# Optimization experiments

Measured on AMD Instinct MI355X. Metric: run time of the kernel, lower is better.

Reference implementation:

```python
import jax, jax.numpy as jnp
import numpy as np

B, T, C = 2, 2048, 1024
H, KH, HD = 16, 4, 64
E, TOPK, I = 8, 2, 1024
GATE = 32
EPS = 1.1920929e-07  # torch F.rms_norm default eps = fp32 machine eps


def rmsnorm(v):
    return v * jax.lax.rsqrt(jnp.mean(v * v, axis=-1, keepdims=True) + EPS)


def rope(v, cos, sin):
    d = v.shape[-1] // 2
    a, b = v[..., :d], v[..., d:]
    return jnp.concatenate([a * cos + b * sin, -a * sin + b * cos], axis=-1)


def setup_inputs() -> dict:
    key = jax.random.key(0)
    ks = jax.random.split(key, 14)
    rn = lambda i, shape, s=1.0: jax.random.normal(ks[i], shape, jnp.float32) * s
    inv_freq = 1.0 / (10000.0 ** (np.arange(HD // 2, dtype=np.float64) / (HD // 2)))
    ang = np.outer(np.arange(T), inv_freq)
    cos = jnp.asarray(np.cos(ang), jnp.float32)[None, :, None, :]
    sin = jnp.asarray(np.sin(ang), jnp.float32)[None, :, None, :]
    w = 0.02
    return {
        'x': rn(0, (B, T, C)),
        've': rn(1, (B, T, KH * HD)),
        'cos': cos,
        'sin': sin,
        'Wq': rn(2, (C, H * HD), w),
        'Wk': rn(3, (KH * HD, C), w),
        'Wv': rn(4, (KH * HD, C), w),
        'Wo': rn(5, (C, C), w),
        've_gate_W': rn(6, (KH, GATE), w),
        'router_W': rn(7, (E, C), w),
        'balance_bias': jnp.zeros((E,), jnp.float32),
        'shared_fc_W': rn(8, (I, C), w),
        'shared_proj_W': rn(9, (C, I), w),
        'exp_fc_W': rn(10, (E, I, C), w),
        'exp_proj_W': rn(11, (E, C, I), w),
        'window_size': T,
    }


def reference(x, ve, cos, sin, Wq, Wk, Wv, Wo, ve_gate_W, router_W, balance_bias,
              shared_fc_W, shared_proj_W, exp_fc_W, exp_proj_W, window_size):
    # ---- attention branch: x = x + attn(norm(x)) ----
    h = rmsnorm(x)
    q = (h @ Wq.T).reshape(B, T, H, HD)
    k = (h @ Wk.T).reshape(B, T, KH, HD)
    v = (h @ Wv.T).reshape(B, T, KH, HD)
    # value-embedding gate (has_ve true for this layer)
    gate = 2.0 * jax.nn.sigmoid(h[..., :GATE] @ ve_gate_W.T)  # [B,T,KH]
    v = v + gate[..., None] * ve.reshape(B, T, KH, HD)
    q, k = rope(q, cos, sin), rope(k, cos, sin)
    q, k = rmsnorm(q), rmsnorm(k)
    g = H // KH
    kr = jnp.repeat(k, g, axis=2)  # GQA expansion [B,T,H,HD]
    vr = jnp.repeat(v, g, axis=2)
    scores = jnp.einsum('bthd,bshd->bhts', q, kr) / jnp.sqrt(jnp.float32(HD))
    ti = jnp.arange(T)[:, None]
    si = jnp.arange(T)[None, :]
    mask = (si <= ti) & (si > ti - window_size)  # causal + sliding window
    scores = jnp.where(mask, scores, -jnp.inf)
    p = jax.nn.softmax(scores, axis=-1)
    y = jnp.einsum('bhts,bshd->bthd', p, vr).reshape(B, T, C)
    x = x + y @ Wo.T

    # ---- MoE branch: x = x + shared(norm(x)) + routed(norm(x)) ----
    h2 = rmsnorm(x)
    shared = jnp.square(jax.nn.relu(h2 @ shared_fc_W.T)) @ shared_proj_W.T
    flat = h2.reshape(-1, C)  # [N,C]
    logits = flat @ router_W.T  # [N,E]
    sc = jax.nn.sigmoid(logits)
    _, topi = jax.lax.top_k(sc + balance_bias, TOPK)  # select on biased scores
    topw = jnp.take_along_axis(sc, topi, axis=1)      # weights from raw scores
    topw = topw / (jnp.sum(topw, axis=-1, keepdims=True) + 1e-20)
    N = flat.shape[0]
    combine = jnp.zeros((N, E), flat.dtype).at[jnp.arange(N)[:, None], topi].add(topw)
    # dense grouped compute, mathematically equal to gather/scatter dispatch
    he = jnp.square(jax.nn.relu(jnp.einsum('nc,eic->eni', flat, exp_fc_W)))
    oe = jnp.einsum('eni,eci->enc', he, exp_proj_W)
    routed = jnp.einsum('enc,ne->nc', oe, combine).reshape(B, T, C)
    return x + shared + routed
```

## Files before the change

### kernel.cpp

```cpp
#include <hip/hip_runtime.h>

#define TT 2048
#define CC 1024
#define NTOK 4096
#define EPSF 1.1920929e-07f

typedef unsigned short u16;
typedef short bf16x8 __attribute__((ext_vector_type(8)));
typedef u16 u16x4 __attribute__((ext_vector_type(4)));
typedef float f32x4 __attribute__((ext_vector_type(4)));

__device__ __forceinline__ u16 f2b(float f) {
  union { float f; unsigned u; } v; v.f = f;
  unsigned r = v.u + 0x7FFFu + ((v.u >> 16) & 1u);
  return (u16)(r >> 16);
}
__device__ __forceinline__ float b2f(u16 u) {
  union { unsigned u; float f; } v; v.u = ((unsigned)u) << 16;
  return v.f;
}
__device__ __forceinline__ void gload16(const u16* g, u16* l) {
  __builtin_amdgcn_global_load_lds(
      (const __attribute__((address_space(1))) void*)g,
      (__attribute__((address_space(3))) void*)l, 16, 0, 0);
}
__device__ __forceinline__ bf16x8 ldsf(const u16* s, int row, int kseg) {
  return *(const bf16x8*)(s + (row << 6) + ((kseg ^ (row & 7)) << 3));
}

__global__ __launch_bounds__(256) void cvt_split4_k(const float* __restrict__ p0,
                                                    const float* __restrict__ p1,
                                                    const float* __restrict__ p2,
                                                    const float* __restrict__ p3,
                                                    u16* __restrict__ h0, u16* __restrict__ l0,
                                                    u16* __restrict__ h1, u16* __restrict__ l1,
                                                    u16* __restrict__ h2, u16* __restrict__ l2,
                                                    u16* __restrict__ h3, u16* __restrict__ l3) {
  const int sizes[4] = {131072, 32768, 32768, 131072};
  int seg = blockIdx.y;
  int i = blockIdx.x * 256 + threadIdx.x;
  if (i >= sizes[seg]) return;
  const float* in = seg == 0 ? p0 : seg == 1 ? p1 : seg == 2 ? p2 : p3;
  u16* ho = seg == 0 ? h0 : seg == 1 ? h1 : seg == 2 ? h2 : h3;
  u16* lo = seg == 0 ? l0 : seg == 1 ? l1 : seg == 2 ? l2 : l3;
  i *= 8;
  float v[8];
  *(float4*)v = *(const float4*)(in + i);
  *(float4*)(v + 4) = *(const float4*)(in + i + 4);
  u16 h[8], l[8];
#pragma unroll
  for (int j = 0; j < 8; ++j) {
    h[j] = f2b(v[j]);
    l[j] = f2b(v[j] - b2f(h[j]));
  }
  *(bf16x8*)(ho + i) = *(bf16x8*)h;
  *(bf16x8*)(lo + i) = *(bf16x8*)l;
}

__global__ __launch_bounds__(256) void rmsnorm_split_k(const float* __restrict__ in,
                                                       u16* __restrict__ hio,
                                                       u16* __restrict__ loo,
                                                       const float* __restrict__ gW,
                                                       float* __restrict__ gates) {
  const int rowi = blockIdx.x;
  const int t = threadIdx.x;
  float4 v = ((const float4*)(in + (size_t)rowi * CC))[t];
  float ss = v.x * v.x + v.y * v.y + v.z * v.z + v.w * v.w;
#pragma unroll
  for (int off = 32; off; off >>= 1) ss += __shfl_down(ss, off, 64);
  __shared__ float red[4];
  __shared__ float hshare[32];
  if ((t & 63) == 0) red[t >> 6] = ss;
  __syncthreads();
  float tot = red[0] + red[1] + red[2] + red[3];
  float sc = rsqrtf(tot * (1.0f / CC) + EPSF);
  float o[4] = {v.x * sc, v.y * sc, v.z * sc, v.w * sc};
  u16 h[4], l[4];
#pragma unroll
  for (int j = 0; j < 4; ++j) {
    h[j] = f2b(o[j]);
    l[j] = f2b(o[j] - b2f(h[j]));
  }
  *(u16x4*)(hio + (size_t)rowi * CC + t * 4) = *(u16x4*)h;
  *(u16x4*)(loo + (size_t)rowi * CC + t * 4) = *(u16x4*)l;
  if (t < 8) *(float4*)&hshare[t << 2] = *(float4*)o;
  __syncthreads();
  if (t < 4) {
    const float* gw = gW + (t << 5);
    float dot = 0.f;
#pragma unroll
    for (int j = 0; j < 32; ++j) dot += hshare[j] * gw[j];
    gates[(rowi << 2) + t] = 2.f / (1.f + __expf(-dot));
  }
}

__global__ __launch_bounds__(256) void rmsnorm_logits_k(const float* __restrict__ in,
                                                        u16* __restrict__ b16o,
                                                        const float* __restrict__ rW,
                                                        float* __restrict__ logits) {
  const int rowi = blockIdx.x;
  const int t = threadIdx.x;
  float4 v = ((const float4*)(in + (size_t)rowi * CC))[t];
  float ss = v.x * v.x + v.y * v.y + v.z * v.z + v.w * v.w;
#pragma unroll
  for (int off = 32; off; off >>= 1) ss += __shfl_down(ss, off, 64);
  __shared__ float red[4];
  __shared__ float red2[8][4];
  if ((t & 63) == 0) red[t >> 6] = ss;
  __syncthreads();
  float tot = red[0] + red[1] + red[2] + red[3];
  float sc = rsqrtf(tot * (1.0f / CC) + EPSF);
  float o[4] = {v.x * sc, v.y * sc, v.z * sc, v.w * sc};
  u16 h[4] = {f2b(o[0]), f2b(o[1]), f2b(o[2]), f2b(o[3])};
  *(u16x4*)(b16o + (size_t)rowi * CC + t * 4) = *(u16x4*)h;
  const float* rwp = rW + (t << 2);
  float part[8];
#pragma unroll
  for (int e = 0; e < 8; ++e) {
    const float* w = rwp + (e << 10);
    part[e] = o[0] * w[0] + o[1] * w[1] + o[2] * w[2] + o[3] * w[3];
  }
  const int wid = t >> 6;
#pragma unroll
  for (int e = 0; e < 8; ++e) {
    float p = part[e];
#pragma unroll
    for (int off = 32; off; off >>= 1) p += __shfl_down(p, off, 64);
    if ((t & 63) == 0) red2[e][wid] = p;
  }
  __syncthreads();
  if (t < 8) logits[rowi * 8 + t] = red2[t][0] + red2[t][1] + red2[t][2] + red2[t][3];
}

template <int MODE>
__global__ __launch_bounds__(256) void gemm_bf_k(
    const u16* __restrict__ A, const u16* __restrict__ A2,
    const u16* __restrict__ Wt, const u16* __restrict__ W2,
    const u16* __restrict__ Wk1, const u16* __restrict__ Wk2,
    const u16* __restrict__ Wv1, const u16* __restrict__ Wv2,
    float* __restrict__ Cf, u16* __restrict__ Cb,
    u16* __restrict__ Ck, u16* __restrict__ Cv,
    const float* __restrict__ addv, int N, int K,
    const int* __restrict__ offsets, const int* __restrict__ counts,
    const int* __restrict__ tok_idx, const float* __restrict__ tok_w,
    const float* __restrict__ cosb, const float* __restrict__ sinb,
    const float* __restrict__ gates, const float* __restrict__ vein) {
  constexpr bool SPLIT = (MODE == 6 || MODE == 11);
  __shared__ __align__(16) u16 Asw[SPLIT ? 16384 : 8192];
  __shared__ __align__(16) u16 Bsw[SPLIT ? 8192 : 4096];
  const int t = threadIdx.x;
  const int lane = t & 63;
  const int l15 = lane & 15, hi = lane >> 4;
  const int wave = t >> 6;
  const int e = blockIdx.z;
  const int mt = blockIdx.y << 7;
  const int bn = blockIdx.x << 6;
  int base = 0, cnt = 0;
  if (MODE == 4 || MODE == 5) {
    cnt = (e == 8) ? NTOK : counts[e];
    if (mt >= cnt) return;
    base = (e == 8) ? 8192 : offsets[e];
  }
  const int r8 = t >> 3;
  const int ksg = (t & 7) ^ (r8 & 7);
  const u16* asrc[4];
  const u16* bsrc[2];
  const u16* asrc2[4];
  const u16* bsrc2[2];
  const u16* W1p = Wt;
  if (MODE == 4 || MODE == 5) W1p = (e == 8) ? Wk1 : Wt + ((size_t)e << 20);
  const u16* W2p = W2;
  int wrow = bn;
  if (MODE == 11) {
    if (bn >= 1280)      { W1p = Wv1; W2p = Wv2; wrow = bn - 1280; }
    else if (bn >= 1024) { W1p = Wk1; W2p = Wk2; wrow = bn - 1024; }
  }
#pragma unroll
  for (int g = 0; g < 4; ++g) {
    int rl = (g << 5) + r8;
    int arow;
    if (MODE == 4) {
      int rr = mt + rl; if (rr > cnt - 1) rr = cnt - 1;
      arow = (e == 8) ? rr : tok_idx[base + rr];
    } else if (MODE == 5) {
      int rr = mt + rl; if (rr > cnt - 1) rr = cnt - 1;
      arow = base + rr;
    } else {
      arow = mt + rl;
    }
    size_t ao = (size_t)arow * K + (ksg << 3);
    asrc[g] = A + ao;
    if (SPLIT) asrc2[g] = A2 + ao;
  }
#pragma unroll
  for (int g = 0; g < 2; ++g) {
    size_t bo = (size_t)(wrow + (g << 5) + r8) * K + (ksg << 3);
    bsrc[g] = W1p + bo;
    if (SPLIT) bsrc2[g] = W2p + bo;
  }
  f32x4 acc[2][4] = {};
  const int nkt = K >> 6;
  for (int kt = 0; kt < nkt; ++kt) {
    __syncthreads();
    const int ko = kt << 6;
#pragma unroll
    for (int g = 0; g < 4; ++g) {
      int co = ((g << 8) + t) << 3;
      gload16(asrc[g] + ko, &Asw[co]);
      if (SPLIT) gload16(asrc2[g] + ko, &Asw[8192 + co]);
    }
#pragma unroll
    for (int g = 0; g < 2; ++g) {
      int co = ((g << 8) + t) << 3;
      gload16(bsrc[g] + ko, &Bsw[co]);
      if (SPLIT) gload16(bsrc2[g] + ko, &Bsw[4096 + co]);
    }
    __syncthreads();
#pragma unroll
    for (int kk = 0; kk < 2; ++kk) {
      bf16x8 ah[2], bh[4];
#pragma unroll
      for (int mi = 0; mi < 2; ++mi)
        ah[mi] = ldsf(Asw, (wave << 5) + (mi << 4) + l15, (kk << 2) + hi);
#pragma unroll
      for (int nj = 0; nj < 4; ++nj)
        bh[nj] = ldsf(Bsw, (nj << 4) + l15, (kk << 2) + hi);
#pragma unroll
      for (int mi = 0; mi < 2; ++mi)
#pragma unroll
        for (int nj = 0; nj < 4; ++nj)
          acc[mi][nj] = __builtin_amdgcn_mfma_f32_16x16x32_bf16(ah[mi], bh[nj], acc[mi][nj], 0, 0, 0);
      if (SPLIT) {
        bf16x8 al[2], bl[4];
#pragma unroll
        for (int mi = 0; mi < 2; ++mi)
          al[mi] = ldsf(Asw + 8192, (wave << 5) + (mi << 4) + l15, (kk << 2) + hi);
#pragma unroll
        for (int nj = 0; nj < 4; ++nj)
          bl[nj] = ldsf(Bsw + 4096, (nj << 4) + l15, (kk << 2) + hi);
#pragma unroll
        for (int mi = 0; mi < 2; ++mi)
#pragma unroll
          for (int nj = 0; nj < 4; ++nj) {
            acc[mi][nj] = __builtin_amdgcn_mfma_f32_16x16x32_bf16(ah[mi], bl[nj], acc[mi][nj], 0, 0, 0);
            acc[mi][nj] = __builtin_amdgcn_mfma_f32_16x16x32_bf16(al[mi], bh[nj], acc[mi][nj], 0, 0, 0);
          }
      }
    }
  }
  if (MODE == 11) {
    if (bn < 1280) {
      u16* outp = (bn < 1024) ? Cb : Ck;
      const int stride = (bn < 1024) ? 1024 : 256;
      const int cbase = (bn < 1024) ? bn : (bn - 1024);
#pragma unroll
      for (int mi = 0; mi < 2; ++mi) {
#pragma unroll
        for (int r = 0; r < 4; ++r) {
          int row = mt + (wave << 5) + (mi << 4) + (hi << 2) + r;
          int tpos = row & (TT - 1);
          const float* cp = cosb + (tpos << 5);
          const float* sp = sinb + (tpos << 5);
          float c0 = cp[l15], s0 = sp[l15];
          float c1 = cp[16 + l15], s1 = sp[16 + l15];
          float a0 = acc[mi][0][r], a1 = acc[mi][1][r];
          float b0 = acc[mi][2][r], b1 = acc[mi][3][r];
          float r00 = a0 * c0 + b0 * s0;
          float r01 = a1 * c1 + b1 * s1;
          float r10 = b0 * c0 - a0 * s0;
          float r11 = b1 * c1 - a1 * s1;
          float ss = r00 * r00 + r01 * r01 + r10 * r10 + r11 * r11;
          ss += __shfl_xor(ss, 1, 64); ss += __shfl_xor(ss, 2, 64);
          ss += __shfl_xor(ss, 4, 64); ss += __shfl_xor(ss, 8, 64);
          float scn = rsqrtf(ss * (1.f / 64.f) + EPSF);
          u16* qp = outp + (size_t)row * stride + cbase;
          qp[l15]      = f2b(r00 * scn);
          qp[16 + l15] = f2b(r01 * scn);
          qp[32 + l15] = f2b(r10 * scn);
          qp[48 + l15] = f2b(r11 * scn);
        }
      }
    } else {
      const int cbase = bn - 1280;
      const int kvh = cbase >> 6;
#pragma unroll
      for (int mi = 0; mi < 2; ++mi) {
#pragma unroll
        for (int r = 0; r < 4; ++r) {
          int row = mt + (wave << 5) + (mi << 4) + (hi << 2) + r;
          float g = gates[(row << 2) + kvh];
          const float* vep = vein + ((size_t)row << 8) + cbase;
          size_t vb_base = ((size_t)(((row >> 11) << 2) + kvh) << 17) + (row & (TT - 1));
#pragma unroll
          for (int nj = 0; nj < 4; ++nj) {
            int d = (nj << 4) + l15;
            Cv[vb_base + ((size_t)d << 11)] = f2b(acc[mi][nj][r] + g * vep[d]);
          }
        }
      }
    }
    return;
  }
#pragma unroll
  for (int mi = 0; mi < 2; ++mi) {
#pragma unroll
    for (int r = 0; r < 4; ++r) {
      int rl = (wave << 5) + (mi << 4) + (hi << 2) + r;
      if (MODE == 4 || MODE == 5) {
        int rr = mt + rl;
        if (rr >= cnt) continue;
        if (MODE == 4) {
          size_t ro = (size_t)(base + rr) * N;
#pragma unroll
          for (int nj = 0; nj < 4; ++nj) {
            float v = acc[mi][nj][r];
            v = v > 0.f ? v * v : 0.f;
            Cb[ro + bn + (nj << 4) + l15] = f2b(v);
          }
        } else {
          int tok = (e == 8) ? rr : tok_idx[base + rr];
          float w = (e == 8) ? 1.0f : tok_w[base + rr];
          size_t ro = (size_t)tok * N;
#pragma unroll
          for (int nj = 0; nj < 4; ++nj)
            atomicAdd(&Cf[ro + bn + (nj << 4) + l15], acc[mi][nj][r] * w);
        }
      } else {
        size_t ro = (size_t)(mt + rl) * N;
        float* outp = (float*)Cb;
#pragma unroll
        for (int nj = 0; nj < 4; ++nj) {
          int col = bn + (nj << 4) + l15;
          float v = acc[mi][nj][r] + addv[ro + col];
          Cf[ro + col] = v;
          outp[ro + col] = v;
        }
      }
    }
  }
}

__global__ __launch_bounds__(256) void attn_mfma_k(const u16* __restrict__ qb,
                                                   const u16* __restrict__ kb,
                                                   const u16* __restrict__ vbT,
                                                   u16* __restrict__ yh,
                                                   u16* __restrict__ yl,
                                                   const int* __restrict__ wszp,
                                                   float* __restrict__ po,
                                                   float* __restrict__ pml,
                                                   const float* __restrict__ cSfc,
                                                   const float* __restrict__ cSproj,
                                                   const float* __restrict__ cEfc,
                                                   const float* __restrict__ cEproj,
                                                   u16* __restrict__ oSfc,
                                                   u16* __restrict__ oSproj,
                                                   u16* __restrict__ oEfc,
                                                   u16* __restrict__ oEproj) {
  const int z = blockIdx.z;
  const int b = z >> 1, seg = z & 1;
  const int kvh = blockIdx.y;
  const int qf = 127 - (int)blockIdx.x;
  const int t = threadIdx.x;
  if (qf < 64 && seg) {
    const int cid = (((b << 2) + kvh) << 6) + ((int)blockIdx.x - 64);
    int chunk = cid * 4608 + t;
#pragma unroll
    for (int it = 0; it < 18; ++it, chunk += 256) {
      const float* in;
      u16* ou;
      int loc;
      if (chunk < 131072)       { in = cSfc;   ou = oSfc;   loc = chunk; }
      else if (chunk < 262144)  { in = cSproj; ou = oSproj; loc = chunk - 131072; }
      else if (chunk < 1310720) { in = cEfc;   ou = oEfc;   loc = chunk - 262144; }
      else                      { in = cEproj; ou = oEproj; loc = chunk - 1310720; }
      size_t i = (size_t)loc * 8;
      float4 a = *(const float4*)(in + i);
      float4 bb = *(const float4*)(in + i + 4);
      u16 r[8] = {f2b(a.x), f2b(a.y), f2b(a.z), f2b(a.w),
                  f2b(bb.x), f2b(bb.y), f2b(bb.z), f2b(bb.w)};
      *(bf16x8*)(ou + i) = *(bf16x8*)r;
    }
    return;
  }
  const int Wn = *wszp;
  const int lane = t & 63, wave = t >> 6;
  const int h = (kvh << 2) + wave;
  const int l15 = lane & 15, hi = lane >> 4;

  __shared__ __align__(16) u16 Klds[2 * 4096];
  __shared__ __align__(16) u16 Vt[2 * 4096];
  __shared__ __align__(16) u16 Plds[4][16 * 64];

  const int qrow0 = qf << 4;
  const int diag = qrow0 >> 6;
  int lo = qrow0 - Wn + 1;
  const int kt0f = lo > 0 ? (lo >> 6) : 0;
  int kt0 = kt0f, ktend = diag;
  if (qf >= 64) {
    int nt = diag - kt0f + 1;
    int mid = kt0f + (nt >> 1);
    if (seg == 0) ktend = mid - 1; else kt0 = mid;
  }

  bf16x8 aQ0, aQ1;
  {
    const u16* qp = qb + ((size_t)((b << 11) + qrow0 + l15) << 10) + (h << 6) + (hi << 3);
    aQ0 = *(const bf16x8*)qp;
    aQ1 = *(const bf16x8*)(qp + 32);
  }
  f32x4 o[4] = {};
  float mrow[4] = {-INFINITY, -INFINITY, -INFINITY, -INFINITY};
  float lrow[4] = {0.f, 0.f, 0.f, 0.f};

  const int kr0 = t >> 3, kc = t & 7;
  const u16* vbase = vbT + ((size_t)((b << 2) + kvh) << 17);

#pragma unroll
  for (int i = 0; i < 2; ++i) {
    int row = kr0 + (i << 5);
    int scol = (kc ^ (row & 7)) << 3;
    gload16(kb + ((size_t)((b << 11) + (kt0 << 6) + row) << 8) + (kvh << 6) + scol,
            &Klds[(t << 3) + (i << 11)]);
    gload16(vbase + ((size_t)row << 11) + (kt0 << 6) + scol,
            &Vt[(t << 3) + (i << 11)]);
  }
  int cur = 0;

  for (int kt = kt0; kt <= ktend; ++kt) {
    __syncthreads();
    if (kt + 1 <= ktend) {
      const int nb = (cur ^ 1) << 12;
#pragma unroll
      for (int i = 0; i < 2; ++i) {
        int row = kr0 + (i << 5);
        int scol = (kc ^ (row & 7)) << 3;
        gload16(kb + ((size_t)((b << 11) + ((kt + 1) << 6) + row) << 8) + (kvh << 6) + scol,
                &Klds[nb + (t << 3) + (i << 11)]);
        gload16(vbase + ((size_t)row << 11) + ((kt + 1) << 6) + scol,
                &Vt[nb + (t << 3) + (i << 11)]);
      }
    }
    const u16* Kb = Klds + (cur << 12);
    const u16* Vb = Vt + (cur << 12);

    float sv[4][4];
    __builtin_amdgcn_s_setprio(1);
#pragma unroll
    for (int kb4 = 0; kb4 < 4; ++kb4) {
      f32x4 S = {0.f, 0.f, 0.f, 0.f};
      bf16x8 B0 = ldsf(Kb, (kb4 << 4) + l15, hi);
      bf16x8 B1 = ldsf(Kb, (kb4 << 4) + l15, 4 + hi);
      S = __builtin_amdgcn_mfma_f32_16x16x32_bf16(aQ0, B0, S, 0, 0, 0);
      S = __builtin_amdgcn_mfma_f32_16x16x32_bf16(aQ1, B1, S, 0, 0, 0);
#pragma unroll
      for (int r = 0; r < 4; ++r) sv[kb4][r] = S[r] * 0.125f;
    }
    __builtin_amdgcn_s_setprio(0);
    if (kt == diag || kt == kt0f) {
#pragma unroll
      for (int kb4 = 0; kb4 < 4; ++kb4) {
        int key = (kt << 6) + (kb4 << 4) + l15;
#pragma unroll
        for (int r = 0; r < 4; ++r) {
          int qg = qrow0 + (hi << 2) + r;
          if (!(key <= qg && key > qg - Wn)) sv[kb4][r] = -INFINITY;
        }
      }
    }

    float scl[4], pv[4][4];
#pragma unroll
    for (int r = 0; r < 4; ++r) {
      float mt2 = fmaxf(fmaxf(sv[0][r], sv[1][r]), fmaxf(sv[2][r], sv[3][r]));
      mt2 = fmaxf(mt2, __shfl_xor(mt2, 1, 64));
      mt2 = fmaxf(mt2, __shfl_xor(mt2, 2, 64));
      mt2 = fmaxf(mt2, __shfl_xor(mt2, 4, 64));
      mt2 = fmaxf(mt2, __shfl_xor(mt2, 8, 64));
      float mn = fmaxf(fmaxf(mrow[r], mt2), -1e30f);
      float sc = __expf(mrow[r] - mn);
      float rs = 0.f;
#pragma unroll
      for (int kb4 = 0; kb4 < 4; ++kb4) {
        float p = __expf(sv[kb4][r] - mn);
        pv[kb4][r] = p;
        rs += p;
      }
      rs += __shfl_xor(rs, 1, 64);
      rs += __shfl_xor(rs, 2, 64);
      rs += __shfl_xor(rs, 4, 64);
      rs += __shfl_xor(rs, 8, 64);
      mrow[r] = mn;
      lrow[r] = lrow[r] * sc + rs;
      scl[r] = sc;
    }

#pragma unroll
    for (int kb4 = 0; kb4 < 4; ++kb4)
#pragma unroll
      for (int r = 0; r < 4; ++r) {
        int row16 = (hi << 2) + r;
        int seg2 = (kb4 << 1) + (l15 >> 3);
        Plds[wave][(row16 << 6) + ((seg2 ^ (row16 & 7)) << 3) + (l15 & 7)] = f2b(pv[kb4][r]);
      }
#pragma unroll
    for (int df = 0; df < 4; ++df) {
      f32x4 t4 = o[df];
      t4[0] *= scl[0]; t4[1] *= scl[1]; t4[2] *= scl[2]; t4[3] *= scl[3];
      o[df] = t4;
    }
    __builtin_amdgcn_s_setprio(1);
#pragma unroll
    for (int ks = 0; ks < 2; ++ks) {
      bf16x8 Ap = ldsf(Plds[wave], l15, (ks << 2) + hi);
#pragma unroll
      for (int df = 0; df < 4; ++df) {
        bf16x8 Bv = ldsf(Vb, (df << 4) + l15, (ks << 2) + hi);
        o[df] = __builtin_amdgcn_mfma_f32_16x16x32_bf16(Ap, Bv, o[df], 0, 0, 0);
      }
    }
    __builtin_amdgcn_s_setprio(0);
    cur ^= 1;
  }

  if (qf < 64) {
    float inv[4];
#pragma unroll
    for (int r = 0; r < 4; ++r) inv[r] = lrow[r] > 0.f ? 1.f / lrow[r] : 0.f;
#pragma unroll
    for (int r = 0; r < 4; ++r) {
      size_t rbase = ((size_t)((b << 11) + qrow0 + (hi << 2) + r) << 10) + (h << 6) + l15;
#pragma unroll
      for (int df = 0; df < 4; ++df) {
        float fo = o[df][r] * inv[r];
        u16 hv = f2b(fo);
        yh[rbase + (df << 4)] = hv;
        yl[rbase + (df << 4)] = f2b(fo - b2f(hv));
      }
    }
  } else {
    const int sidx = (b << 1) + seg;
    const int prow0 = qrow0 - 1024;
#pragma unroll
    for (int r = 0; r < 4; ++r) {
      size_t pbase = ((size_t)(sidx * 1024 + prow0 + (hi << 2) + r) << 10) + (h << 6) + l15;
#pragma unroll
      for (int df = 0; df < 4; ++df) po[pbase + (df << 4)] = o[df][r];
    }
    if (l15 == 0) {
#pragma unroll
      for (int r = 0; r < 4; ++r) {
        size_t mb = ((size_t)(sidx * 1024 + prow0 + (hi << 2) + r) << 5) + (h << 1);
        pml[mb] = mrow[r];
        pml[mb + 1] = lrow[r];
      }
    }
  }
}

__global__ __launch_bounds__(256) void combine_k(const float* __restrict__ po,
                                                 const float* __restrict__ pml,
                                                 u16* __restrict__ yh,
                                                 u16* __restrict__ yl) {
  const int prow = blockIdx.x, b = blockIdx.y;
  const int t = threadIdx.x;
  const int h = t >> 4, d0 = (t & 15) << 2;
  const int s0 = b << 1, s1 = s0 + 1;
  size_t i0 = ((size_t)(s0 * 1024 + prow) << 5) + (h << 1);
  size_t i1 = ((size_t)(s1 * 1024 + prow) << 5) + (h << 1);
  float m0 = pml[i0], l0 = pml[i0 + 1];
  float m1 = pml[i1], l1 = pml[i1 + 1];
  float m = fmaxf(m0, m1);
  float sc0 = __expf(m0 - m), sc1 = __expf(m1 - m);
  float l = l0 * sc0 + l1 * sc1;
  float inv = l > 0.f ? 1.f / l : 0.f;
  size_t o0 = ((size_t)(s0 * 1024 + prow) << 10) + (h << 6) + d0;
  size_t o1 = ((size_t)(s1 * 1024 + prow) << 10) + (h << 6) + d0;
  float4 a = *(const float4*)&po[o0];
  float4 c = *(const float4*)&po[o1];
  float y0 = (a.x * sc0 + c.x * sc1) * inv;
  float y1 = (a.y * sc0 + c.y * sc1) * inv;
  float y2 = (a.z * sc0 + c.z * sc1) * inv;
  float y3 = (a.w * sc0 + c.w * sc1) * inv;
  u16 hv[4] = {f2b(y0), f2b(y1), f2b(y2), f2b(y3)};
  u16 lv[4] = {f2b(y0 - b2f(hv[0])), f2b(y1 - b2f(hv[1])),
               f2b(y2 - b2f(hv[2])), f2b(y3 - b2f(hv[3]))};
  size_t rbase = ((size_t)((b << 11) + 1024 + prow) << 10) + (h << 6) + d0;
  *(u16x4*)(yh + rbase) = *(u16x4*)hv;
  *(u16x4*)(yl + rbase) = *(u16x4*)lv;
}

__global__ __launch_bounds__(256) void topk_k(const float* __restrict__ logits,
                                              const float* __restrict__ bias,
                                              int* __restrict__ topi,
                                              float* __restrict__ topw,
                                              int* __restrict__ counts) {
  int n = blockIdx.x * 256 + threadIdx.x;
  if (n >= NTOK) return;
  float sc[8], sel[8];
#pragma unroll
  for (int e2 = 0; e2 < 8; ++e2) {
    float sg = 1.f / (1.f + __expf(-logits[n * 8 + e2]));
    sc[e2] = sg;
    sel[e2] = sg + bias[e2];
  }
  int i1 = 0; float b1 = sel[0];
#pragma unroll
  for (int j = 1; j < 8; ++j) if (sel[j] > b1) { b1 = sel[j]; i1 = j; }
  int i2 = -1; float b2 = -INFINITY;
#pragma unroll
  for (int j = 0; j < 8; ++j) if (j != i1 && sel[j] > b2) { b2 = sel[j]; i2 = j; }
  float w1 = sc[i1], w2 = sc[i2];
  float invs = 1.f / (w1 + w2 + 1e-20f);
  topi[n * 2] = i1; topi[n * 2 + 1] = i2;
  topw[n * 2] = w1 * invs; topw[n * 2 + 1] = w2 * invs;
  atomicAdd(&counts[i1], 1);
  atomicAdd(&counts[i2], 1);
}

__global__ void scan_k(const int* __restrict__ counts, int* __restrict__ offsets) {
  if (threadIdx.x == 0 && blockIdx.x == 0) {
    int s = 0;
    for (int e2 = 0; e2 < 8; ++e2) { offsets[e2] = s; s += counts[e2]; }
    offsets[8] = s;
  }
}

__global__ __launch_bounds__(256) void scatter_k(const int* __restrict__ topi,
                                                 const float* __restrict__ topw,
                                                 const int* __restrict__ offsets,
                                                 int* __restrict__ counts2,
                                                 int* __restrict__ tok_idx,
                                                 float* __restrict__ tok_w) {
  int n = blockIdx.x * 256 + threadIdx.x;
  if (n >= NTOK) return;
  for (int kk = 0; kk < 2; ++kk) {
    int e2 = topi[n * 2 + kk];
    int slot = atomicAdd(&counts2[e2], 1);
    int p = offsets[e2] + slot;
    tok_idx[p] = n;
    tok_w[p] = topw[n * 2 + kk];
  }
}

extern "C" void kernel_launch(void* const* d_in, const int* in_sizes, int n_in,
                              void* d_out, int out_size, void* d_ws, size_t ws_size,
                              hipStream_t stream) {
  const float* x = (const float*)d_in[0];
  const float* ve = (const float*)d_in[1];
  const float* cosb = (const float*)d_in[2];
  const float* sinb = (const float*)d_in[3];
  const float* Wq = (const float*)d_in[4];
  const float* Wk = (const float*)d_in[5];
  const float* Wv = (const float*)d_in[6];
  const float* Wo = (const float*)d_in[7];
  const float* gW = (const float*)d_in[8];
  const float* routerW = (const float*)d_in[9];
  const float* bias = (const float*)d_in[10];
  const float* Wsfc = (const float*)d_in[11];
  const float* Wsproj = (const float*)d_in[12];
  const float* Wefc = (const float*)d_in[13];
  const float* Weproj = (const float*)d_in[14];
  const int* wsz = (const int*)d_in[15];
  float* out = (float*)d_out;
  char* WS = (char*)d_ws;

  u16* Wefc_b   = (u16*)(WS + 0);
  u16* Weproj_b = (u16*)(WS + 16777216);
  u16* Wsfc_b   = (u16*)(WS + 33554432);
  u16* Wsproj_b = (u16*)(WS + 35651584);
  u16* Wq_hi    = (u16*)(WS + 37748736);
  u16* Wq_lo    = (u16*)(WS + 39845888);
  u16* Wk_hi    = (u16*)(WS + 41943040);
  u16* Wk_lo    = (u16*)(WS + 42467328);
  u16* Wv_hi    = (u16*)(WS + 42991616);
  u16* Wv_lo    = (u16*)(WS + 43515904);
  u16* Wo_hi    = (u16*)(WS + 44040192);
  u16* Wo_lo    = (u16*)(WS + 46137344);
  u16* h_hi     = (u16*)(WS + 48234496);
  u16* h_lo     = (u16*)(WS + 56623104);
  u16* qb       = (u16*)(WS + 65011712);
  u16* kb       = (u16*)(WS + 73400320);
  u16* vb       = (u16*)(WS + 75497472);
  u16* y_hi     = (u16*)(WS + 77594624);
  u16* y_lo     = (u16*)(WS + 85983232);
  float* po     = (float*)(WS + 48234496);
  float* x2     = (float*)(WS + 48234496);
  u16* h2_b     = (u16*)(WS + 85983232);
  u16* he_b     = (u16*)(WS + 48234496);
  float* gates  = (float*)(WS + 94371840);
  float* logits = (float*)(WS + 94437376);
  int* meta     = (int*)(WS + 94568448);
  int* counts   = meta;
  int* counts2  = meta + 8;
  int* offsets  = meta + 16;
  int* topi     = meta + 32;
  float* topw   = (float*)(meta + 8224);
  int* tok_idx  = meta + 16416;
  float* tok_w  = (float*)(meta + 24608);
  float* pml    = (float*)(WS + 94703616);

  hipMemsetAsync(counts, 0, 16 * sizeof(int), stream);

  cvt_split4_k<<<dim3(512, 4), 256, 0, stream>>>(Wq, Wk, Wv, Wo,
      Wq_hi, Wq_lo, Wk_hi, Wk_lo, Wv_hi, Wv_lo, Wo_hi, Wo_lo);

  rmsnorm_split_k<<<NTOK, 256, 0, stream>>>(x, h_hi, h_lo, gW, gates);
  gemm_bf_k<11><<<dim3(24, 32), 256, 0, stream>>>(
      h_hi, h_lo, Wq_hi, Wq_lo, Wk_hi, Wk_lo, Wv_hi, Wv_lo,
      nullptr, qb, kb, vb, nullptr, 1536, 1024,
      nullptr, nullptr, nullptr, nullptr, cosb, sinb, gates, ve);
  attn_mfma_k<<<dim3(128, 4, 4), 256, 0, stream>>>(qb, kb, vb, y_hi, y_lo, wsz, po, pml,
      Wsfc, Wsproj, Wefc, Weproj, Wsfc_b, Wsproj_b, Wefc_b, Weproj_b);
  combine_k<<<dim3(1024, 2), 256, 0, stream>>>(po, pml, y_hi, y_lo);
  gemm_bf_k<6><<<dim3(16, 32), 256, 0, stream>>>(
      y_hi, y_lo, Wo_hi, Wo_lo, nullptr, nullptr, nullptr, nullptr,
      x2, (u16*)out, nullptr, nullptr, x, 1024, 1024,
      nullptr, nullptr, nullptr, nullptr, nullptr, nullptr, nullptr, nullptr);
  rmsnorm_logits_k<<<NTOK, 256, 0, stream>>>(x2, h2_b, routerW, logits);
  topk_k<<<16, 256, 0, stream>>>(logits, bias, topi, topw, counts);
  scan_k<<<1, 64, 0, stream>>>(counts, offsets);
  scatter_k<<<16, 256, 0, stream>>>(topi, topw, offsets, counts2, tok_idx, tok_w);
  gemm_bf_k<4><<<dim3(16, 32, 9), 256, 0, stream>>>(
      h2_b, nullptr, Wefc_b, nullptr, Wsfc_b, nullptr, nullptr, nullptr,
      nullptr, he_b, nullptr, nullptr, nullptr, 1024, 1024,
      offsets, counts, tok_idx, nullptr, nullptr, nullptr, nullptr, nullptr);
  gemm_bf_k<5><<<dim3(16, 32, 9), 256, 0, stream>>>(
      he_b, nullptr, Weproj_b, nullptr, Wsproj_b, nullptr, nullptr, nullptr,
      out, nullptr, nullptr, nullptr, nullptr, 1024, 1024,
      offsets, counts, tok_idx, tok_w, nullptr, nullptr, nullptr, nullptr);
}
```

Baseline: 390.4 us.

## Fuse weight split-conversion into rmsnorm launch and halve M-tile for split GEMMs

The separate fp32-to-bf16 hi/lo weight conversion kernel is merged into the rmsnorm kernel as extra blocks, removing one launch and letting the two independent jobs run concurrently. For the split-precision GEMMs (QKV with RoPE and the Wo projection), the M tile shrinks from 128 to 64 rows, so each wave computes one 16-row MFMA slice and the grid doubles. This is meant to raise occupancy and CU coverage for these small GEMMs (768 and 512 blocks before), at the cost of less reuse of the B tile per block.

```diff
diff --git a/kernel.cpp b/kernel.cpp
--- a/kernel.cpp
+++ b/kernel.cpp
@@ -28,42 +28,43 @@
   return *(const bf16x8*)(s + (row << 6) + ((kseg ^ (row & 7)) << 3));
 }
 
-__global__ __launch_bounds__(256) void cvt_split4_k(const float* __restrict__ p0,
-                                                    const float* __restrict__ p1,
-                                                    const float* __restrict__ p2,
-                                                    const float* __restrict__ p3,
-                                                    u16* __restrict__ h0, u16* __restrict__ l0,
-                                                    u16* __restrict__ h1, u16* __restrict__ l1,
-                                                    u16* __restrict__ h2, u16* __restrict__ l2,
-                                                    u16* __restrict__ h3, u16* __restrict__ l3) {
-  const int sizes[4] = {131072, 32768, 32768, 131072};
-  int seg = blockIdx.y;
-  int i = blockIdx.x * 256 + threadIdx.x;
-  if (i >= sizes[seg]) return;
-  const float* in = seg == 0 ? p0 : seg == 1 ? p1 : seg == 2 ? p2 : p3;
-  u16* ho = seg == 0 ? h0 : seg == 1 ? h1 : seg == 2 ? h2 : h3;
-  u16* lo = seg == 0 ? l0 : seg == 1 ? l1 : seg == 2 ? l2 : l3;
-  i *= 8;
-  float v[8];
-  *(float4*)v = *(const float4*)(in + i);
-  *(float4*)(v + 4) = *(const float4*)(in + i + 4);
-  u16 h[8], l[8];
-#pragma unroll
-  for (int j = 0; j < 8; ++j) {
-    h[j] = f2b(v[j]);
-    l[j] = f2b(v[j] - b2f(h[j]));
-  }
-  *(bf16x8*)(ho + i) = *(bf16x8*)h;
-  *(bf16x8*)(lo + i) = *(bf16x8*)l;
-}
-
 __global__ __launch_bounds__(256) void rmsnorm_split_k(const float* __restrict__ in,
                                                        u16* __restrict__ hio,
                                                        u16* __restrict__ loo,
                                                        const float* __restrict__ gW,
-                                                       float* __restrict__ gates) {
-  const int rowi = blockIdx.x;
+                                                       float* __restrict__ gates,
+                                                       const float* __restrict__ p0,
+                                                       const float* __restrict__ p1,
+                                                       const float* __restrict__ p2,
+                                                       const float* __restrict__ p3,
+                                                       u16* __restrict__ h0, u16* __restrict__ l0,
+                                                       u16* __restrict__ h1, u16* __restrict__ l1,
+                                                       u16* __restrict__ h2, u16* __restrict__ l2,
+                                                       u16* __restrict__ h3, u16* __restrict__ l3) {
+  const int bid = blockIdx.x;
   const int t = threadIdx.x;
+  if (bid >= NTOK) {
+    int chunk = (bid - NTOK) * 256 + t;
+    const float* inw; u16* ho; u16* lo2; int loc;
+    if (chunk < 131072)      { inw = p0; ho = h0; lo2 = l0; loc = chunk; }
+    else if (chunk < 163840) { inw = p1; ho = h1; lo2 = l1; loc = chunk - 131072; }
+    else if (chunk < 196608) { inw = p2; ho = h2; lo2 = l2; loc = chunk - 163840; }
+    else                     { inw = p3; ho = h3; lo2 = l3; loc = chunk - 196608; }
+    size_t i = (size_t)loc * 8;
+    float v[8];
+    *(float4*)v = *(const float4*)(inw + i);
+    *(float4*)(v + 4) = *(const float4*)(inw + i + 4);
+    u16 hh[8], ll[8];
+#pragma unroll
+    for (int j = 0; j < 8; ++j) {
+      hh[j] = f2b(v[j]);
+      ll[j] = f2b(v[j] - b2f(hh[j]));
+    }
+    *(bf16x8*)(ho + i) = *(bf16x8*)hh;
+    *(bf16x8*)(lo2 + i) = *(bf16x8*)ll;
+    return;
+  }
+  const int rowi = bid;
   float4 v = ((const float4*)(in + (size_t)rowi * CC))[t];
   float ss = v.x * v.x + v.y * v.y + v.z * v.z + v.w * v.w;
 #pragma unroll
@@ -146,14 +147,16 @@
     const float* __restrict__ cosb, const float* __restrict__ sinb,
     const float* __restrict__ gates, const float* __restrict__ vein) {
   constexpr bool SPLIT = (MODE == 6 || MODE == 11);
-  __shared__ __align__(16) u16 Asw[SPLIT ? 16384 : 8192];
+  constexpr int NAG = SPLIT ? 2 : 4;
+  constexpr int NMI = SPLIT ? 1 : 2;
+  __shared__ __align__(16) u16 Asw[8192];
   __shared__ __align__(16) u16 Bsw[SPLIT ? 8192 : 4096];
   const int t = threadIdx.x;
   const int lane = t & 63;
   const int l15 = lane & 15, hi = lane >> 4;
   const int wave = t >> 6;
   const int e = blockIdx.z;
-  const int mt = blockIdx.y << 7;
+  const int mt = blockIdx.y << (SPLIT ? 6 : 7);
   const int bn = blockIdx.x << 6;
   int base = 0, cnt = 0;
   if (MODE == 4 || MODE == 5) {
@@ -163,9 +166,9 @@
   }
   const int r8 = t >> 3;
   const int ksg = (t & 7) ^ (r8 & 7);
-  const u16* asrc[4];
+  const u16* asrc[NAG];
   const u16* bsrc[2];
-  const u16* asrc2[4];
+  const u16* asrc2[NAG];
   const u16* bsrc2[2];
   const u16* W1p = Wt;
   if (MODE == 4 || MODE == 5) W1p = (e == 8) ? Wk1 : Wt + ((size_t)e << 20);
@@ -176,7 +179,7 @@
     else if (bn >= 1024) { W1p = Wk1; W2p = Wk2; wrow = bn - 1024; }
   }
 #pragma unroll
-  for (int g = 0; g < 4; ++g) {
+  for (int g = 0; g < NAG; ++g) {
     int rl = (g << 5) + r8;
     int arow;
     if (MODE == 4) {
@@ -198,16 +201,16 @@
     bsrc[g] = W1p + bo;
     if (SPLIT) bsrc2[g] = W2p + bo;
   }
-  f32x4 acc[2][4] = {};
+  f32x4 acc[NMI][4] = {};
   const int nkt = K >> 6;
   for (int kt = 0; kt < nkt; ++kt) {
     __syncthreads();
     const int ko = kt << 6;
 #pragma unroll
-    for (int g = 0; g < 4; ++g) {
+    for (int g = 0; g < NAG; ++g) {
       int co = ((g << 8) + t) << 3;
       gload16(asrc[g] + ko, &Asw[co]);
-      if (SPLIT) gload16(asrc2[g] + ko, &Asw[8192 + co]);
+      if (SPLIT) gload16(asrc2[g] + ko, &Asw[4096 + co]);
     }
 #pragma unroll
     for (int g = 0; g < 2; ++g) {
@@ -218,28 +221,28 @@
     __syncthreads();
 #pragma unroll
     for (int kk = 0; kk < 2; ++kk) {
-      bf16x8 ah[2], bh[4];
-#pragma unroll
-      for (int mi = 0; mi < 2; ++mi)
-        ah[mi] = ldsf(Asw, (wave << 5) + (mi << 4) + l15, (kk << 2) + hi);
+      bf16x8 ah[NMI], bh[4];
+#pragma unroll
+      for (int mi = 0; mi < NMI; ++mi)
+        ah[mi] = ldsf(Asw, (SPLIT ? (wave << 4) : ((wave << 5) + (mi << 4))) + l15, (kk << 2) + hi);
 #pragma unroll
       for (int nj = 0; nj < 4; ++nj)
         bh[nj] = ldsf(Bsw, (nj << 4) + l15, (kk << 2) + hi);
 #pragma unroll
-      for (int mi = 0; mi < 2; ++mi)
+      for (int mi = 0; mi < NMI; ++mi)
 #pragma unroll
         for (int nj = 0; nj < 4; ++nj)
           acc[mi][nj] = __builtin_amdgcn_mfma_f32_16x16x32_bf16(ah[mi], bh[nj], acc[mi][nj], 0, 0, 0);
       if (SPLIT) {
-        bf16x8 al[2], bl[4];
-#pragma unroll
-        for (int mi = 0; mi < 2; ++mi)
-          al[mi] = ldsf(Asw + 8192, (wave << 5) + (mi << 4) + l15, (kk << 2) + hi);
+        bf16x8 al[NMI], bl[4];
+#pragma unroll
+        for (int mi = 0; mi < NMI; ++mi)
+          al[mi] = ldsf(Asw + 4096, (wave << 4) + l15, (kk << 2) + hi);
 #pragma unroll
         for (int nj = 0; nj < 4; ++nj)
           bl[nj] = ldsf(Bsw + 4096, (nj << 4) + l15, (kk << 2) + hi);
 #pragma unroll
-        for (int mi = 0; mi < 2; ++mi)
+        for (int mi = 0; mi < NMI; ++mi)
 #pragma unroll
           for (int nj = 0; nj < 4; ++nj) {
             acc[mi][nj] = __builtin_amdgcn_mfma_f32_16x16x32_bf16(ah[mi], bl[nj], acc[mi][nj], 0, 0, 0);
@@ -254,58 +257,52 @@
       const int stride = (bn < 1024) ? 1024 : 256;
       const int cbase = (bn < 1024) ? bn : (bn - 1024);
 #pragma unroll
-      for (int mi = 0; mi < 2; ++mi) {
-#pragma unroll
-        for (int r = 0; r < 4; ++r) {
-          int row = mt + (wave << 5) + (mi << 4) + (hi << 2) + r;
-          int tpos = row & (TT - 1);
-          const float* cp = cosb + (tpos << 5);
-          const float* sp = sinb + (tpos << 5);
-          float c0 = cp[l15], s0 = sp[l15];
-          float c1 = cp[16 + l15], s1 = sp[16 + l15];
-          float a0 = acc[mi][0][r], a1 = acc[mi][1][r];
-          float b0 = acc[mi][2][r], b1 = acc[mi][3][r];
-          float r00 = a0 * c0 + b0 * s0;
-          float r01 = a1 * c1 + b1 * s1;
-          float r10 = b0 * c0 - a0 * s0;
-          float r11 = b1 * c1 - a1 * s1;
-          float ss = r00 * r00 + r01 * r01 + r10 * r10 + r11 * r11;
-          ss += __shfl_xor(ss, 1, 64); ss += __shfl_xor(ss, 2, 64);
-          ss += __shfl_xor(ss, 4, 64); ss += __shfl_xor(ss, 8, 64);
-          float scn = rsqrtf(ss * (1.f / 64.f) + EPSF);
-          u16* qp = outp + (size_t)row * stride + cbase;
-          qp[l15]      = f2b(r00 * scn);
-          qp[16 + l15] = f2b(r01 * scn);
-          qp[32 + l15] = f2b(r10 * scn);
-          qp[48 + l15] = f2b(r11 * scn);
-        }
+      for (int r = 0; r < 4; ++r) {
+        int row = mt + (wave << 4) + (hi << 2) + r;
+        int tpos = row & (TT - 1);
+        const float* cp = cosb + (tpos << 5);
+        const float* sp = sinb + (tpos << 5);
+        float c0 = cp[l15], s0 = sp[l15];
+        float c1 = cp[16 + l15], s1 = sp[16 + l15];
+        float a0 = acc[0][0][r], a1 = acc[0][1][r];
+        float b0 = acc[0][2][r], b1 = acc[0][3][r];
+        float r00 = a0 * c0 + b0 * s0;
+        float r01 = a1 * c1 + b1 * s1;
+        float r10 = b0 * c0 - a0 * s0;
+        float r11 = b1 * c1 - a1 * s1;
+        float ss = r00 * r00 + r01 * r01 + r10 * r10 + r11 * r11;
+        ss += __shfl_xor(ss, 1, 64); ss += __shfl_xor(ss, 2, 64);
+        ss += __shfl_xor(ss, 4, 64); ss += __shfl_xor(ss, 8, 64);
+        float scn = rsqrtf(ss * (1.f / 64.f) + EPSF);
+        u16* qp = outp + (size_t)row * stride + cbase;
+        qp[l15]      = f2b(r00 * scn);
+        qp[16 + l15] = f2b(r01 * scn);
+        qp[32 + l15] = f2b(r10 * scn);
+        qp[48 + l15] = f2b(r11 * scn);
       }
     } else {
       const int cbase = bn - 1280;
       const int kvh = cbase >> 6;
 #pragma unroll
-      for (int mi = 0; mi < 2; ++mi) {
-#pragma unroll
-        for (int r = 0; r < 4; ++r) {
-          int row = mt + (wave << 5) + (mi << 4) + (hi << 2) + r;
-          float g = gates[(row << 2) + kvh];
-          const float* vep = vein + ((size_t)row << 8) + cbase;
-          size_t vb_base = ((size_t)(((row >> 11) << 2) + kvh) << 17) + (row & (TT - 1));
-#pragma unroll
-          for (int nj = 0; nj < 4; ++nj) {
-            int d = (nj << 4) + l15;
-            Cv[vb_base + ((size_t)d << 11)] = f2b(acc[mi][nj][r] + g * vep[d]);
-          }
+      for (int r = 0; r < 4; ++r) {
+        int row = mt + (wave << 4) + (hi << 2) + r;
+        float g = gates[(row << 2) + kvh];
+        const float* vep = vein + ((size_t)row << 8) + cbase;
+        size_t vb_base = ((size_t)(((row >> 11) << 2) + kvh) << 17) + (row & (TT - 1));
+#pragma unroll
+        for (int nj = 0; nj < 4; ++nj) {
+          int d = (nj << 4) + l15;
+          Cv[vb_base + ((size_t)d << 11)] = f2b(acc[0][nj][r] + g * vep[d]);
         }
       }
     }
     return;
   }
 #pragma unroll
-  for (int mi = 0; mi < 2; ++mi) {
+  for (int mi = 0; mi < NMI; ++mi) {
 #pragma unroll
     for (int r = 0; r < 4; ++r) {
-      int rl = (wave << 5) + (mi << 4) + (hi << 2) + r;
+      int rl = (SPLIT ? (wave << 4) : ((wave << 5) + (mi << 4))) + (hi << 2) + r;
       if (MODE == 4 || MODE == 5) {
         int rr = mt + rl;
         if (rr >= cnt) continue;
@@ -701,18 +698,17 @@
 
   hipMemsetAsync(counts, 0, 16 * sizeof(int), stream);
 
-  cvt_split4_k<<<dim3(512, 4), 256, 0, stream>>>(Wq, Wk, Wv, Wo,
+  rmsnorm_split_k<<<NTOK + 1280, 256, 0, stream>>>(x, h_hi, h_lo, gW, gates,
+      Wq, Wk, Wv, Wo,
       Wq_hi, Wq_lo, Wk_hi, Wk_lo, Wv_hi, Wv_lo, Wo_hi, Wo_lo);
-
-  rmsnorm_split_k<<<NTOK, 256, 0, stream>>>(x, h_hi, h_lo, gW, gates);
-  gemm_bf_k<11><<<dim3(24, 32), 256, 0, stream>>>(
+  gemm_bf_k<11><<<dim3(24, 64), 256, 0, stream>>>(
       h_hi, h_lo, Wq_hi, Wq_lo, Wk_hi, Wk_lo, Wv_hi, Wv_lo,
       nullptr, qb, kb, vb, nullptr, 1536, 1024,
       nullptr, nullptr, nullptr, nullptr, cosb, sinb, gates, ve);
   attn_mfma_k<<<dim3(128, 4, 4), 256, 0, stream>>>(qb, kb, vb, y_hi, y_lo, wsz, po, pml,
       Wsfc, Wsproj, Wefc, Weproj, Wsfc_b, Wsproj_b, Wefc_b, Weproj_b);
   combine_k<<<dim3(1024, 2), 256, 0, stream>>>(po, pml, y_hi, y_lo);
-  gemm_bf_k<6><<<dim3(16, 32), 256, 0, stream>>>(
+  gemm_bf_k<6><<<dim3(16, 64), 256, 0, stream>>>(
       y_hi, y_lo, Wo_hi, Wo_lo, nullptr, nullptr, nullptr, nullptr,
       x2, (u16*)out, nullptr, nullptr, x, 1024, 1024,
       nullptr, nullptr, nullptr, nullptr, nullptr, nullptr, nullptr, nullptr);
```

New measurement: 395.6 us. No clear change (+1.3%).
